# Performance work log

Hardware: AMD Instinct MI355X
Metric: run time of the kernel (lower is better)

Reference implementation:

```python
import jax, jax.numpy as jnp
import numpy as np

D_MODEL = 1024
NHEAD = 16
HEAD_DIM = D_MODEL // NHEAD
DFF = 4096
EPS = 1e-5


def _layernorm(x, g, b):
    mu = jnp.mean(x, axis=-1, keepdims=True)
    var = jnp.mean(jnp.square(x - mu), axis=-1, keepdims=True)
    return (x - mu) * jax.lax.rsqrt(var + EPS) * g + b


def setup_inputs() -> dict:
    key = jax.random.key(0)
    ks = jax.random.split(key, 20)
    B, S = 2, 2048
    s = 0.02
    inp = {
        "src": jax.random.normal(ks[0], (B, S, D_MODEL), jnp.float32),
        "recompute_idx": jnp.sort(jax.random.randint(ks[1], (409,), 0, S)),
        "cached_k": jax.random.normal(ks[2], (B, NHEAD, S, HEAD_DIM), jnp.float32),
        "cached_v": jax.random.normal(ks[3], (B, NHEAD, S, HEAD_DIM), jnp.float32),
        "Wq": jax.random.normal(ks[4], (D_MODEL, D_MODEL), jnp.float32) * s,
        "bq": jnp.zeros((D_MODEL,), jnp.float32),
        "Wk": jax.random.normal(ks[5], (D_MODEL, D_MODEL), jnp.float32) * s,
        "bk": jnp.zeros((D_MODEL,), jnp.float32),
        "Wv": jax.random.normal(ks[6], (D_MODEL, D_MODEL), jnp.float32) * s,
        "bv": jnp.zeros((D_MODEL,), jnp.float32),
        "Wo": jax.random.normal(ks[7], (D_MODEL, D_MODEL), jnp.float32) * s,
        "bo": jnp.zeros((D_MODEL,), jnp.float32),
        "W1": jax.random.normal(ks[8], (DFF, D_MODEL), jnp.float32) * s,
        "b1": jnp.zeros((DFF,), jnp.float32),
        "W2": jax.random.normal(ks[9], (D_MODEL, DFF), jnp.float32) * s,
        "b2": jnp.zeros((D_MODEL,), jnp.float32),
        "g1": jnp.ones((D_MODEL,), jnp.float32),
        "beta1": jnp.zeros((D_MODEL,), jnp.float32),
        "g2": jnp.ones((D_MODEL,), jnp.float32),
        "beta2": jnp.zeros((D_MODEL,), jnp.float32),
    }
    return inp


def reference(src, recompute_idx, cached_k, cached_v, Wq, bq, Wk, bk, Wv, bv,
              Wo, bo, W1, b1, W2, b2, g1, beta1, g2, beta2):
    B, S, D = src.shape
    H, hd = NHEAD, HEAD_DIM

    # Q for all tokens
    q = (src @ Wq.T + bq).reshape(B, S, H, hd).transpose(0, 2, 1, 3)  # [B,H,S,hd]

    # K/V recomputed only for selected tokens, scattered over cached KV
    src_rec = src[:, recompute_idx, :]  # [B,R,D]
    R = src_rec.shape[1]
    k_rec = (src_rec @ Wk.T + bk).reshape(B, R, H, hd).transpose(0, 2, 1, 3)
    v_rec = (src_rec @ Wv.T + bv).reshape(B, R, H, hd).transpose(0, 2, 1, 3)
    k_full = cached_k.at[:, :, recompute_idx, :].set(k_rec)  # [B,H,S,hd]
    v_full = cached_v.at[:, :, recompute_idx, :].set(v_rec)

    # attention over mixed cached/fresh KV
    scores = jnp.einsum('bhqd,bhkd->bhqk', q, k_full) / np.sqrt(hd).astype(src.dtype)
    probs = jax.nn.softmax(scores, axis=-1)
    attn = jnp.einsum('bhqk,bhkd->bhqd', probs, v_full)
    attn = attn.transpose(0, 2, 1, 3).reshape(B, S, D)
    attn = attn @ Wo.T + bo

    x = _layernorm(src + attn, g1, beta1)
    ff = jax.nn.relu(x @ W1.T + b1) @ W2.T + b2
    x = _layernorm(x + ff, g2, beta2)
    return x
```

## Files before the change

kernel.cpp:

```cpp
#include <hip/hip_runtime.h>
#include <hip/hip_bf16.h>

typedef __attribute__((ext_vector_type(4))) float f32x4;
typedef __attribute__((ext_vector_type(8))) short s16x8;
typedef __attribute__((ext_vector_type(4))) short s16x4;
typedef __attribute__((ext_vector_type(2))) short s16x2;

typedef __attribute__((address_space(1))) const unsigned int guint;
typedef __attribute__((address_space(3))) unsigned int luint;

#define D_MODEL 1024
#define NHEAD 16
#define HEAD_DIM 64
#define DFF 4096
#define SEQ 2048
#define BATCH 2
#define QSCALE 0.18033688011112042f

__device__ __forceinline__ float b2f(short s) {
  union { unsigned int u; float f; } v;
  v.u = ((unsigned int)(unsigned short)s) << 16;
  return v.f;
}
__device__ __forceinline__ short f2b(float f) {
  __hip_bfloat16 h = __float2bfloat16(f);
  return *reinterpret_cast<short*>(&h);
}
__device__ __forceinline__ s16x8 cvt8(f32x4 a, f32x4 b) {
  s16x8 r;
  #pragma unroll
  for (int i = 0; i < 4; ++i) { r[i] = f2b(a[i]); r[i + 4] = f2b(b[i]); }
  return r;
}

template<int MODE, int BN, bool AF32, bool WF32>
__global__ __launch_bounds__(256, 3)
void gemm_nt(const void* __restrict__ Av, const void* __restrict__ Wv,
             const float* __restrict__ bias, short* __restrict__ out,
             int M, int N, int K,
             const int* __restrict__ idx, int R,
             const float* __restrict__ bias2, const float* __restrict__ bias3,
             short* __restrict__ pB, short* __restrict__ pC,
             short* __restrict__ pD)
{
  constexpr bool GLDS = (!AF32 && !WF32);
  constexpr int NI = BN / 32;

  const float* Af = (const float*)Av;
  const short* Ab = (const short*)Av;
  const float* Wf = (const float*)Wv;
  const short* Wb = (const short*)Wv;

  const int tid  = threadIdx.x;
  const int lane = tid & 63, wave = tid >> 6;
  const int g = lane >> 4, l15 = lane & 15;
  const int wm = (wave & 1) * 64, wn = (wave >> 1) * (BN / 2);

  const int nwg = gridDim.x * gridDim.y;
  int lid = blockIdx.y * gridDim.x + blockIdx.x;
  if ((nwg & 7) == 0) lid = (lid & 7) * (nwg >> 3) + (lid >> 3);
  const int bn = lid % gridDim.x;
  const int bm0 = lid / gridDim.x;

  int task = 0, bm = bm0, Mt = M;
  if (MODE == 8) {
    if (bm0 < 32)      { task = 0; bm = bm0;      Mt = M; }
    else if (bm0 < 39) { task = 1; bm = bm0 - 32; Mt = BATCH * R; }
    else               { task = 2; bm = bm0 - 39; Mt = BATCH * R; }
  }

  f32x4 acc[4][NI] = {};

  if constexpr (GLDS) {
    __shared__ short As[2][128][32];
    __shared__ short Bs[2][BN][32];

    const short* Wbase = Wb + ((MODE == 8) ? ((size_t)task << 20) : 0);
    const int nz   = (MODE == 6) ? gridDim.z : 1;
    const int Keff = K / nz;
    const int kOff = (MODE == 6) ? (int)blockIdx.z * Keff : 0;

    const int rA0 = wave * 16 + (lane >> 2);
    const int rA1 = rA0 + 64;
    const int c0  = (lane & 3) * 8;

    auto arow = [&](int r) -> long {
      const int gm = bm * 128 + r;
      const int am = gm < Mt ? gm : Mt - 1;
      if (MODE == 8 && task > 0) {
        const int b0 = am / R;
        return (long)(b0 * SEQ + idx[am - b0 * R]);
      }
      return am;
    };
    const long aR0 = arow(rA0), aR1 = arow(rA1);
    const long wR0 = (long)bn * BN + rA0;

    const short* gA0 = Ab + aR0 * K + kOff + c0;
    const short* gA1 = Ab + aR1 * K + kOff + c0;
    const short* gB0 = Wbase + wR0 * K + kOff + c0;
    const short* gB1 = nullptr;
    if constexpr (BN == 128) gB1 = Wbase + ((long)bn * BN + rA1) * K + kOff + c0;

    auto stage = [&](int buf, int k0) {
      luint* lA0 = (luint*)((short*)As + buf * 4096 + wave * 512);
      luint* lA1 = (luint*)((short*)As + buf * 4096 + (4 + wave) * 512);
      luint* lB0 = (luint*)((short*)Bs + buf * (BN * 32) + wave * 512);
      __builtin_amdgcn_global_load_lds((guint*)(gA0 + k0), lA0, 16, 0, 0);
      __builtin_amdgcn_global_load_lds((guint*)(gA1 + k0), lA1, 16, 0, 0);
      __builtin_amdgcn_global_load_lds((guint*)(gB0 + k0), lB0, 16, 0, 0);
      if constexpr (BN == 128) {
        luint* lB1 = (luint*)((short*)Bs + buf * (BN * 32) + (4 + wave) * 512);
        __builtin_amdgcn_global_load_lds((guint*)(gB1 + k0), lB1, 16, 0, 0);
      }
    };

    stage(0, 0);
    __syncthreads();
    int cur = 0;
    for (int k0 = 0; k0 < Keff; k0 += 32) {
      const int k1 = k0 + 32;
      if (k1 < Keff) stage(cur ^ 1, k1);

      s16x8 af[4], bf4[NI];
      #pragma unroll
      for (int mi = 0; mi < 4; ++mi)
        af[mi] = *(const s16x8*)&As[cur][wm + mi * 16 + l15][g * 8];
      #pragma unroll
      for (int ni = 0; ni < NI; ++ni)
        bf4[ni] = *(const s16x8*)&Bs[cur][wn + ni * 16 + l15][g * 8];
      #pragma unroll
      for (int mi = 0; mi < 4; ++mi)
        #pragma unroll
        for (int ni = 0; ni < NI; ++ni)
          acc[mi][ni] = __builtin_amdgcn_mfma_f32_16x16x32_bf16(af[mi], bf4[ni], acc[mi][ni], 0, 0, 0);

      __syncthreads();
      cur ^= 1;
    }
  } else {
    __shared__ short As[128][40];
    __shared__ short Bs[128][40];
    const int r0 = tid >> 1, c0 = (tid & 1) * 16;
    const int gm0 = bm * 128 + r0;
    const int am0 = gm0 < M ? gm0 : M - 1;
    long aRow0;
    if (MODE == 3 || MODE == 4) {
      const int b0 = am0 / R;
      aRow0 = (long)(b0 * SEQ + idx[am0 - b0 * R]);
    } else {
      aRow0 = am0;
    }
    const long wRow0 = bn * 128 + r0;

    for (int k0 = 0; k0 < K; k0 += 32) {
      __syncthreads();
      if (AF32) {
        f32x4 a0 = *(const f32x4*)(Af + aRow0 * K + k0 + c0);
        f32x4 a1 = *(const f32x4*)(Af + aRow0 * K + k0 + c0 + 4);
        f32x4 a2 = *(const f32x4*)(Af + aRow0 * K + k0 + c0 + 8);
        f32x4 a3 = *(const f32x4*)(Af + aRow0 * K + k0 + c0 + 12);
        *(s16x8*)&As[r0][c0]     = cvt8(a0, a1);
        *(s16x8*)&As[r0][c0 + 8] = cvt8(a2, a3);
      } else {
        *(s16x8*)&As[r0][c0]     = *(const s16x8*)(Ab + aRow0 * K + k0 + c0);
        *(s16x8*)&As[r0][c0 + 8] = *(const s16x8*)(Ab + aRow0 * K + k0 + c0 + 8);
      }
      if (WF32) {
        f32x4 w0 = *(const f32x4*)(Wf + wRow0 * K + k0 + c0);
        f32x4 w1 = *(const f32x4*)(Wf + wRow0 * K + k0 + c0 + 4);
        f32x4 w2 = *(const f32x4*)(Wf + wRow0 * K + k0 + c0 + 8);
        f32x4 w3 = *(const f32x4*)(Wf + wRow0 * K + k0 + c0 + 12);
        *(s16x8*)&Bs[r0][c0]     = cvt8(w0, w1);
        *(s16x8*)&Bs[r0][c0 + 8] = cvt8(w2, w3);
      } else {
        *(s16x8*)&Bs[r0][c0]     = *(const s16x8*)(Wb + wRow0 * K + k0 + c0);
        *(s16x8*)&Bs[r0][c0 + 8] = *(const s16x8*)(Wb + wRow0 * K + k0 + c0 + 8);
      }
      __syncthreads();

      s16x8 af[4], bf4[4];
      #pragma unroll
      for (int mi = 0; mi < 4; ++mi)
        af[mi] = *(const s16x8*)&As[wm + mi * 16 + l15][g * 8];
      #pragma unroll
      for (int ni = 0; ni < 4; ++ni)
        bf4[ni] = *(const s16x8*)&Bs[wn + ni * 16 + l15][g * 8];
      #pragma unroll
      for (int mi = 0; mi < 4; ++mi)
        #pragma unroll
        for (int ni = 0; ni < 4; ++ni)
          acc[mi][ni % NI] = __builtin_amdgcn_mfma_f32_16x16x32_bf16(af[mi], bf4[ni], acc[mi][ni % NI], 0, 0, 0);
    }
  }

  short* outz = out;
  if (MODE == 6) {
    const int z = blockIdx.z;
    outz = (z == 0) ? out : (z == 1) ? pB : (z == 2) ? pC : pD;
  }

  #pragma unroll
  for (int mi = 0; mi < 4; ++mi) {
    #pragma unroll
    for (int ni = 0; ni < NI; ++ni) {
      const int gn = bn * BN + wn + ni * 16 + l15;
      float bv;
      if (MODE == 6)      bv = 0.f;
      else if (MODE == 8) bv = (task == 0) ? bias[gn] : (task == 1) ? bias2[gn] : bias3[gn];
      else                bv = bias[gn];
      #pragma unroll
      for (int r = 0; r < 4; ++r) {
        const int gm = bm * 128 + wm + mi * 16 + g * 4 + r;
        if (MODE == 8) { if (gm >= Mt) continue; }
        else           { if (gm >= M)  continue; }
        float v = acc[mi][ni][r] + bv;
        if (MODE == 1) v = v > 0.f ? v : 0.f;
        if (MODE == 2) v *= QSCALE;
        if (MODE == 0 || MODE == 1) {
          out[(long)gm * N + gn] = f2b(v);
        } else if (MODE == 2) {
          const int b = gm >> 11, s = gm & (SEQ - 1);
          const int h = gn >> 6, d = gn & 63;
          out[(((long)(b * NHEAD + h)) * SEQ + s) * 64 + d] = f2b(v);
        } else if (MODE == 3) {
          const int b = gm / R, s = idx[gm - b * R];
          const int h = gn >> 6, d = gn & 63;
          out[(((long)(b * NHEAD + h)) * SEQ + s) * 64 + d] = f2b(v);
        } else if (MODE == 4) {
          const int b = gm / R, s = idx[gm - b * R];
          const int h = gn >> 6, d = gn & 63;
          out[(((long)(b * NHEAD + h)) * 64 + d) * SEQ + s] = f2b(v);
        } else if (MODE == 6) {
          outz[(long)gm * N + gn] = f2b(v);
        } else {
          const int h = gn >> 6, d = gn & 63;
          if (task == 0) {
            const int b = gm >> 11, s = gm & (SEQ - 1);
            out[(((long)(b * NHEAD + h)) * SEQ + s) * 64 + d] = f2b(v * QSCALE);
          } else if (task == 1) {
            const int b = gm / R, s = idx[gm - b * R];
            (out + (1L << 22))[(((long)(b * NHEAD + h)) * SEQ + s) * 64 + d] = f2b(v);
          } else {
            const int b = gm / R, s = idx[gm - b * R];
            (out + (1L << 23))[(((long)(b * NHEAD + h)) * 64 + d) * SEQ + s] = f2b(v);
          }
        }
      }
    }
  }
}

__global__ __launch_bounds__(256, 2)
void attn_fwd(const short* __restrict__ Q, const short* __restrict__ Kf,
              const short* __restrict__ Vt, short* __restrict__ out)
{
  __shared__ short Kl[2][64][64];
  __shared__ short Vl[2][64][64];

  const int tid  = threadIdx.x;
  const int lane = tid & 63, w = tid >> 6;
  const int g = lane >> 4, l15 = lane & 15;
  const int bh = blockIdx.x;
  const int qt = blockIdx.y;
  const int b  = bh >> 4, h = bh & 15;

  const long base = (long)bh * SEQ * 64;
  const int  q0   = qt * 128 + w * 32;

  s16x8 qf[2][2];
  #pragma unroll
  for (int mi = 0; mi < 2; ++mi)
    #pragma unroll
    for (int c = 0; c < 2; ++c)
      qf[mi][c] = *(const s16x8*)(Q + base + (long)(q0 + mi * 16 + l15) * 64 + c * 32 + g * 8);

  f32x4 o[2][4] = {};
  f32x4 os[2] = {};

  s16x8 ones;
  #pragma unroll
  for (int j = 0; j < 8; ++j) ones[j] = (short)0x3F80;

  auto ldsw = [](short (*buf)[64], int row, int slot) -> short* {
    return (short*)((char*)&buf[0][0] + row * 128 + ((slot ^ (row & 7)) << 4));
  };

  const int bo0 = w * 2048 + lane * 16;
  const int bo1 = bo0 + 1024;
  const int row0 = bo0 >> 7, ss0 = (((bo0 >> 4) & 7) ^ (row0 & 7));
  const int row1 = bo1 >> 7, ss1 = (((bo1 >> 4) & 7) ^ (row1 & 7));
  const short* gK0 = Kf + base + row0 * 64 + ss0 * 8;
  const short* gK1 = Kf + base + row1 * 64 + ss1 * 8;
  const short* gV0 = Vt + base + (long)row0 * SEQ + ss0 * 8;
  const short* gV1 = Vt + base + (long)row1 * SEQ + ss1 * 8;

  auto stage = [&](int buf, int t) {
    char* kb8 = (char*)&Kl[buf][0][0] + w * 2048;
    char* vb8 = (char*)&Vl[buf][0][0] + w * 2048;
    __builtin_amdgcn_global_load_lds((guint*)(gK0 + t * 4096), (luint*)kb8, 16, 0, 0);
    __builtin_amdgcn_global_load_lds((guint*)(gK1 + t * 4096), (luint*)(kb8 + 1024), 16, 0, 0);
    __builtin_amdgcn_global_load_lds((guint*)(gV0 + t * 64), (luint*)vb8, 16, 0, 0);
    __builtin_amdgcn_global_load_lds((guint*)(gV1 + t * 64), (luint*)(vb8 + 1024), 16, 0, 0);
  };

  stage(0, 0);
  __syncthreads();
  int cur = 0;
  for (int t = 0; t < SEQ / 64; ++t) {
    if (t + 1 < SEQ / 64) stage(cur ^ 1, t + 1);

    f32x4 sc[2][4] = {};
    __builtin_amdgcn_s_setprio(1);
    #pragma unroll
    for (int c = 0; c < 2; ++c)
      #pragma unroll
      for (int n = 0; n < 4; ++n) {
        s16x8 kb = *(const s16x8*)ldsw(Kl[cur], n * 16 + l15, c * 4 + g);
        sc[0][n] = __builtin_amdgcn_mfma_f32_16x16x32_bf16(kb, qf[0][c], sc[0][n], 0, 0, 0);
        sc[1][n] = __builtin_amdgcn_mfma_f32_16x16x32_bf16(kb, qf[1][c], sc[1][n], 0, 0, 0);
      }
    __builtin_amdgcn_s_setprio(0);

    s16x8 pa[2][2];
    #pragma unroll
    for (int mi = 0; mi < 2; ++mi) {
      #pragma unroll
      for (int n = 0; n < 4; ++n)
        #pragma unroll
        for (int r = 0; r < 4; ++r) {
          float e;
          asm("v_exp_f32 %0, %1" : "=v"(e) : "v"(sc[mi][n][r]));
          sc[mi][n][r] = e;
        }
      unsigned int wpk[4][2];
      #pragma unroll
      for (int n = 0; n < 4; ++n)
        #pragma unroll
        for (int p = 0; p < 2; ++p)
          asm("v_cvt_pk_bf16_f32 %0, %1, %2"
              : "=v"(wpk[n][p]) : "v"(sc[mi][n][2 * p]), "v"(sc[mi][n][2 * p + 1]));
      #pragma unroll
      for (int c = 0; c < 2; ++c) {
        union { s16x8 v; unsigned int u[4]; } pu;
        #pragma unroll
        for (int p = 0; p < 2; ++p) {
          unsigned int a = wpk[2 * c][p], bb = wpk[2 * c + 1][p];
          asm volatile("v_permlane32_swap_b32 %0, %1" : "+v"(a), "+v"(bb));
          asm volatile("v_permlane16_swap_b32 %0, %1" : "+v"(a), "+v"(bb));
          pu.u[p]     = a;
          pu.u[2 + p] = bb;
        }
        pa[mi][c] = pu.v;
      }
    }

    __builtin_amdgcn_s_setprio(1);
    #pragma unroll
    for (int dt = 0; dt < 4; ++dt)
      #pragma unroll
      for (int c = 0; c < 2; ++c) {
        s16x8 vb = *(const s16x8*)ldsw(Vl[cur], dt * 16 + l15, c * 4 + g);
        o[0][dt] = __builtin_amdgcn_mfma_f32_16x16x32_bf16(pa[0][c], vb, o[0][dt], 0, 0, 0);
        o[1][dt] = __builtin_amdgcn_mfma_f32_16x16x32_bf16(pa[1][c], vb, o[1][dt], 0, 0, 0);
      }
    #pragma unroll
    for (int mi = 0; mi < 2; ++mi)
      #pragma unroll
      for (int c = 0; c < 2; ++c)
        os[mi] = __builtin_amdgcn_mfma_f32_16x16x32_bf16(pa[mi][c], ones, os[mi], 0, 0, 0);
    __builtin_amdgcn_s_setprio(0);

    __syncthreads();
    cur ^= 1;
  }

  float inv[2][4];
  #pragma unroll
  for (int mi = 0; mi < 2; ++mi)
    #pragma unroll
    for (int r = 0; r < 4; ++r)
      inv[mi][r] = 1.0f / os[mi][r];

  #pragma unroll
  for (int mi = 0; mi < 2; ++mi)
    #pragma unroll
    for (int dt = 0; dt < 4; ++dt)
      #pragma unroll
      for (int r = 0; r < 4; ++r) {
        const int q   = q0 + mi * 16 + g * 4 + r;
        const int col = h * 64 + dt * 16 + l15;
        out[((long)(b * SEQ + q)) * D_MODEL + col] = f2b(o[mi][dt][r] * inv[mi][r]);
      }
}

template<bool RES_F32, bool OUT_F32>
__global__ __launch_bounds__(256, 4)
void ln_ff2(const short* __restrict__ p0, const short* __restrict__ p1,
            const float* __restrict__ bias, const void* __restrict__ resv,
            const float* __restrict__ g, const float* __restrict__ beta,
            void* __restrict__ outv)
{
  __shared__ float red[8];
  const int row = blockIdx.x;
  const int tid = threadIdx.x;
  const int lane = tid & 63, w = tid >> 6;

  s16x4 v0 = *(const s16x4*)(p0 + (long)row * D_MODEL + tid * 4);
  s16x4 v1 = *(const s16x4*)(p1 + (long)row * D_MODEL + tid * 4);
  f32x4 vb = *(const f32x4*)(bias + tid * 4);
  float x[4];
  if (RES_F32) {
    f32x4 vr = *(const f32x4*)((const float*)resv + (long)row * D_MODEL + tid * 4);
    #pragma unroll
    for (int i = 0; i < 4; ++i) x[i] = vr[i] + b2f(v0[i]) + b2f(v1[i]) + vb[i];
  } else {
    s16x4 vr = *(const s16x4*)((const short*)resv + (long)row * D_MODEL + tid * 4);
    #pragma unroll
    for (int i = 0; i < 4; ++i) x[i] = b2f(vr[i]) + b2f(v0[i]) + b2f(v1[i]) + vb[i];
  }

  float sum = x[0] + x[1] + x[2] + x[3];
  #pragma unroll
  for (int msk = 32; msk >= 1; msk >>= 1) sum += __shfl_xor(sum, msk, 64);
  if (lane == 0) red[w] = sum;
  __syncthreads();
  sum = red[0] + red[1] + red[2] + red[3];
  const float mu = sum * (1.f / D_MODEL);

  float sq = 0.f;
  #pragma unroll
  for (int i = 0; i < 4; ++i) { float d = x[i] - mu; sq += d * d; }
  #pragma unroll
  for (int msk = 32; msk >= 1; msk >>= 1) sq += __shfl_xor(sq, msk, 64);
  if (lane == 0) red[4 + w] = sq;
  __syncthreads();
  sq = red[4] + red[5] + red[6] + red[7];
  const float rs = rsqrtf(sq * (1.f / D_MODEL) + 1e-5f);

  if (OUT_F32) {
    f32x4 ov;
    #pragma unroll
    for (int i = 0; i < 4; ++i) {
      const int c = tid * 4 + i;
      ov[i] = (x[i] - mu) * rs * g[c] + beta[c];
    }
    *(f32x4*)((float*)outv + (long)row * D_MODEL + tid * 4) = ov;
  } else {
    s16x4 ov;
    #pragma unroll
    for (int i = 0; i < 4; ++i) {
      const int c = tid * 4 + i;
      ov[i] = f2b((x[i] - mu) * rs * g[c] + beta[c]);
    }
    *(s16x4*)((short*)outv + (long)row * D_MODEL + tid * 4) = ov;
  }
}

__global__ __launch_bounds__(256, 4)
void ln_ff4(const short* __restrict__ p0, const short* __restrict__ p1,
            const short* __restrict__ p2, const short* __restrict__ p3,
            const float* __restrict__ bias, const short* __restrict__ xres,
            const float* __restrict__ g, const float* __restrict__ beta,
            float* __restrict__ outv)
{
  __shared__ float red[8];
  const int row = blockIdx.x;
  const int tid = threadIdx.x;
  const int lane = tid & 63, w = tid >> 6;

  s16x4 v0 = *(const s16x4*)(p0 + (long)row * D_MODEL + tid * 4);
  s16x4 v1 = *(const s16x4*)(p1 + (long)row * D_MODEL + tid * 4);
  s16x4 v2 = *(const s16x4*)(p2 + (long)row * D_MODEL + tid * 4);
  s16x4 v3 = *(const s16x4*)(p3 + (long)row * D_MODEL + tid * 4);
  s16x4 vx = *(const s16x4*)(xres + (long)row * D_MODEL + tid * 4);
  f32x4 vb = *(const f32x4*)(bias + tid * 4);
  float x[4];
  #pragma unroll
  for (int i = 0; i < 4; ++i)
    x[i] = b2f(vx[i]) + b2f(v0[i]) + b2f(v1[i]) + b2f(v2[i]) + b2f(v3[i]) + vb[i];

  float sum = x[0] + x[1] + x[2] + x[3];
  #pragma unroll
  for (int msk = 32; msk >= 1; msk >>= 1) sum += __shfl_xor(sum, msk, 64);
  if (lane == 0) red[w] = sum;
  __syncthreads();
  sum = red[0] + red[1] + red[2] + red[3];
  const float mu = sum * (1.f / D_MODEL);

  float sq = 0.f;
  #pragma unroll
  for (int i = 0; i < 4; ++i) { float d = x[i] - mu; sq += d * d; }
  #pragma unroll
  for (int msk = 32; msk >= 1; msk >>= 1) sq += __shfl_xor(sq, msk, 64);
  if (lane == 0) red[4 + w] = sq;
  __syncthreads();
  sq = red[4] + red[5] + red[6] + red[7];
  const float rs = rsqrtf(sq * (1.f / D_MODEL) + 1e-5f);

  f32x4 ov;
  #pragma unroll
  for (int i = 0; i < 4; ++i) {
    const int c = tid * 4 + i;
    ov[i] = (x[i] - mu) * rs * g[c] + beta[c];
  }
  *(f32x4*)(outv + (long)row * D_MODEL + tid * 4) = ov;
}

template<bool RES_F32, bool OUT_F32>
__global__ __launch_bounds__(256, 4)
void ln_res(const short* __restrict__ a, const void* __restrict__ resv,
            const float* __restrict__ g, const float* __restrict__ beta,
            void* __restrict__ outv)
{
  __shared__ float red[8];
  const int row = blockIdx.x;
  const int tid = threadIdx.x;
  const int lane = tid & 63, w = tid >> 6;

  s16x4 va = *(const s16x4*)(a + (long)row * D_MODEL + tid * 4);
  float x[4];
  if (RES_F32) {
    f32x4 vr = *(const f32x4*)((const float*)resv + (long)row * D_MODEL + tid * 4);
    #pragma unroll
    for (int i = 0; i < 4; ++i) x[i] = b2f(va[i]) + vr[i];
  } else {
    s16x4 vr = *(const s16x4*)((const short*)resv + (long)row * D_MODEL + tid * 4);
    #pragma unroll
    for (int i = 0; i < 4; ++i) x[i] = b2f(va[i]) + b2f(vr[i]);
  }
  float sum = x[0] + x[1] + x[2] + x[3];
  #pragma unroll
  for (int msk = 32; msk >= 1; msk >>= 1) sum += __shfl_xor(sum, msk, 64);
  if (lane == 0) red[w] = sum;
  __syncthreads();
  sum = red[0] + red[1] + red[2] + red[3];
  const float mu = sum * (1.f / D_MODEL);

  float sq = 0.f;
  #pragma unroll
  for (int i = 0; i < 4; ++i) { float d = x[i] - mu; sq += d * d; }
  #pragma unroll
  for (int msk = 32; msk >= 1; msk >>= 1) sq += __shfl_xor(sq, msk, 64);
  if (lane == 0) red[4 + w] = sq;
  __syncthreads();
  sq = red[4] + red[5] + red[6] + red[7];
  const float rs = rsqrtf(sq * (1.f / D_MODEL) + 1e-5f);

  if (OUT_F32) {
    f32x4 ov;
    #pragma unroll
    for (int i = 0; i < 4; ++i) {
      const int c = tid * 4 + i;
      ov[i] = (x[i] - mu) * rs * g[c] + beta[c];
    }
    *(f32x4*)((float*)outv + (long)row * D_MODEL + tid * 4) = ov;
  } else {
    s16x4 ov;
    #pragma unroll
    for (int i = 0; i < 4; ++i) {
      const int c = tid * 4 + i;
      ov[i] = f2b((x[i] - mu) * rs * g[c] + beta[c]);
    }
    *(s16x4*)((short*)outv + (long)row * D_MODEL + tid * 4) = ov;
  }
}

__global__ void cvt_all(const float* __restrict__ ck, const float* __restrict__ cv,
                        const float* __restrict__ src,
                        const float* __restrict__ Wq, const float* __restrict__ Wk,
                        const float* __restrict__ Wv, const float* __restrict__ Wo,
                        const float* __restrict__ W1, const float* __restrict__ W2,
                        short* __restrict__ k_ws, short* __restrict__ v_ws,
                        short* __restrict__ srcb,
                        short* __restrict__ Wqb, short* __restrict__ W1b,
                        short* __restrict__ W2b)
{
  for (int i = blockIdx.x * blockDim.x + threadIdx.x; i < 5767168;
       i += gridDim.x * blockDim.x) {
    if (i >= 5242880) {
      const int j = i - 5242880;
      const int bh = j >> 14;
      const int rem = j & 16383;
      const int d = rem & 63;
      const int s0 = (rem >> 6) << 3;
      s16x8 r;
      #pragma unroll
      for (int k = 0; k < 8; ++k)
        r[k] = f2b(cv[((long)bh * SEQ + s0 + k) * 64 + d]);
      *(s16x8*)(v_ws + ((long)bh * 64 + d) * SEQ + s0) = r;
      continue;
    }
    const float* s; short* d; int li;
    if      (i < 1048576) { s = ck;  d = k_ws;           li = i; }
    else if (i < 2097152) { s = src; d = srcb;           li = i - 1048576; }
    else if (i < 2359296) { s = Wq;  d = Wqb;            li = i - 2097152; }
    else if (i < 2621440) { s = Wk;  d = Wqb + 1048576;  li = i - 2359296; }
    else if (i < 2883584) { s = Wv;  d = Wqb + 2097152;  li = i - 2621440; }
    else if (i < 3145728) { s = Wo;  d = Wqb + 3145728;  li = i - 2883584; }
    else if (i < 4194304) { s = W1;  d = W1b;            li = i - 3145728; }
    else                  { s = W2;  d = W2b;            li = i - 4194304; }
    f32x4 v = *(const f32x4*)(s + (long)li * 4);
    s16x4 r;
    #pragma unroll
    for (int j = 0; j < 4; ++j) r[j] = f2b(v[j]);
    *(s16x4*)(d + (long)li * 4) = r;
  }
}

__global__ void cvt_v_t(const float* __restrict__ in, short* __restrict__ out)
{
  const int c2 = blockIdx.x * blockDim.x + threadIdx.x;
  const int bh = c2 >> 14;
  const int rem = c2 & 16383;
  const int d = rem & 63;
  const int s0 = (rem >> 6) << 3;
  s16x8 r;
  #pragma unroll
  for (int j = 0; j < 8; ++j)
    r[j] = f2b(in[((long)bh * SEQ + s0 + j) * 64 + d]);
  *(s16x8*)(out + ((long)bh * 64 + d) * SEQ + s0) = r;
}

__global__ void cvt_f32_bf16(const f32x4* __restrict__ in, s16x4* __restrict__ out, int n4)
{
  for (int i = blockIdx.x * blockDim.x + threadIdx.x; i < n4; i += gridDim.x * blockDim.x) {
    f32x4 v = in[i];
    s16x4 r;
    #pragma unroll
    for (int j = 0; j < 4; ++j) r[j] = f2b(v[j]);
    out[i] = r;
  }
}

extern "C" void kernel_launch(void* const* d_in, const int* in_sizes, int n_in,
                              void* d_out, int out_size, void* d_ws, size_t ws_size,
                              hipStream_t stream)
{
  const float* src = (const float*)d_in[0];
  const int*   idx = (const int*)  d_in[1];
  const float* ck  = (const float*)d_in[2];
  const float* cv  = (const float*)d_in[3];
  const float* Wq  = (const float*)d_in[4];
  const float* bq  = (const float*)d_in[5];
  const float* Wk  = (const float*)d_in[6];
  const float* bk  = (const float*)d_in[7];
  const float* Wv  = (const float*)d_in[8];
  const float* bv  = (const float*)d_in[9];
  const float* Wo  = (const float*)d_in[10];
  const float* bo  = (const float*)d_in[11];
  const float* W1  = (const float*)d_in[12];
  const float* b1  = (const float*)d_in[13];
  const float* W2  = (const float*)d_in[14];
  const float* b2  = (const float*)d_in[15];
  const float* g1  = (const float*)d_in[16];
  const float* be1 = (const float*)d_in[17];
  const float* g2  = (const float*)d_in[18];
  const float* be2 = (const float*)d_in[19];
  float* out = (float*)d_out;

  char* ws = (char*)d_ws;
  const size_t SZ = (size_t)4096 * 1024 * 2;
  short* x_ws    = (short*)(ws);
  short* proj_ws = (short*)(ws + SZ);
  short* q_ws    = (short*)(ws + 2 * SZ);
  short* k_ws    = (short*)(ws + 3 * SZ);
  short* v_ws    = (short*)(ws + 4 * SZ);
  short* attn_ws = (short*)(ws + 5 * SZ);
  short* h_ws    = (short*)(ws + 2 * SZ);
  short* W1b     = (short*)(ws + 6 * SZ);
  short* W2b     = (short*)(ws + 7 * SZ);
  short* srcb    = (short*)(ws + 8 * SZ);
  short* Wqb     = (short*)(ws + 9 * SZ);
  const bool big = ws_size >= 10 * SZ;

  const int M = BATCH * SEQ;
  const int R = 409;
  const int Mr = BATCH * R;
  const int nkv4 = BATCH * NHEAD * SEQ * HEAD_DIM / 4;

  if (big) {
    cvt_all<<<2048, 256, 0, stream>>>(ck, cv, src, Wq, Wk, Wv, Wo, W1, W2,
                                      k_ws, v_ws, srcb, Wqb, W1b, W2b);
    gemm_nt<8, 64, false, false><<<dim3(16, 46), 256, 0, stream>>>(
        srcb, Wqb, bq, q_ws, M, 1024, 1024, idx, R, bk, bv, nullptr, nullptr, nullptr);
    attn_fwd<<<dim3(BATCH * NHEAD, SEQ / 128), 256, 0, stream>>>(q_ws, k_ws, v_ws, attn_ws);
    gemm_nt<6, 64, false, false><<<dim3(16, 32, 2), 256, 0, stream>>>(
        attn_ws, Wqb + 3145728, nullptr, proj_ws, M, 1024, 1024, nullptr, 0,
        nullptr, nullptr, q_ws, nullptr, nullptr);
    ln_ff2<true, false><<<4096, 256, 0, stream>>>(proj_ws, q_ws, bo, src, g1, be1, x_ws);
    gemm_nt<1, 128, false, false><<<dim3(32, 32), 256, 0, stream>>>(
        x_ws, W1b, b1, h_ws, M, DFF, 1024, nullptr, 0, nullptr, nullptr,
        nullptr, nullptr, nullptr);
    gemm_nt<6, 128, false, false><<<dim3(8, 32, 4), 256, 0, stream>>>(
        h_ws, W2b, nullptr, proj_ws, M, 1024, 4096, nullptr, 0,
        nullptr, nullptr, W1b, srcb, Wqb);
    ln_ff4<<<4096, 256, 0, stream>>>(proj_ws, W1b, srcb, Wqb, b2, x_ws, g2, be2, out);
  } else {
    cvt_f32_bf16<<<2048, 256, 0, stream>>>((const f32x4*)ck, (s16x4*)k_ws, nkv4);
    cvt_v_t<<<2048, 256, 0, stream>>>(cv, v_ws);
    gemm_nt<2, 128, true, true><<<dim3(8, 32), 256, 0, stream>>>(
        src, Wq, bq, q_ws, M, 1024, 1024, nullptr, 0, nullptr, nullptr, nullptr, nullptr, nullptr);
    gemm_nt<3, 128, true, true><<<dim3(8, 7), 256, 0, stream>>>(
        src, Wk, bk, k_ws, Mr, 1024, 1024, idx, R, nullptr, nullptr, nullptr, nullptr, nullptr);
    gemm_nt<4, 128, true, true><<<dim3(8, 7), 256, 0, stream>>>(
        src, Wv, bv, v_ws, Mr, 1024, 1024, idx, R, nullptr, nullptr, nullptr, nullptr, nullptr);
    attn_fwd<<<dim3(BATCH * NHEAD, SEQ / 128), 256, 0, stream>>>(q_ws, k_ws, v_ws, attn_ws);
    gemm_nt<0, 128, false, true><<<dim3(8, 32), 256, 0, stream>>>(
        attn_ws, Wo, bo, proj_ws, M, 1024, 1024, nullptr, 0, nullptr, nullptr, nullptr, nullptr, nullptr);
    ln_res<true, false><<<4096, 256, 0, stream>>>(proj_ws, src, g1, be1, x_ws);
    gemm_nt<1, 128, false, true><<<dim3(32, 32), 256, 0, stream>>>(
        x_ws, W1, b1, h_ws, M, DFF, 1024, nullptr, 0, nullptr, nullptr, nullptr, nullptr, nullptr);
    gemm_nt<0, 128, false, true><<<dim3(8, 32), 256, 0, stream>>>(
        h_ws, W2, b2, proj_ws, M, 1024, DFF, nullptr, 0, nullptr, nullptr, nullptr, nullptr, nullptr);
    ln_res<false, true><<<4096, 256, 0, stream>>>(proj_ws, x_ws, g2, be2, out);
  }
}
```

Measured before the change: 236.9 us.

## Swizzle GEMM LDS tiles and use partial vmcnt waits for double-buffer prefetch

In the GEMM kernel the global-to-LDS column placement is XOR-swizzled and the MFMA fragment reads use the matching swizzled column, so LDS reads should hit fewer bank conflicts. In both the GEMM and attention loops, the full __syncthreads after each prefetch is replaced by an explicit s_waitcnt vmcnt(N) plus s_barrier. Only the current tile's loads are waited on, while the next tile's loads stay in flight during compute. This relies on exact counts of outstanding loads per thread; a wrong count would give stale-data races.

```diff
diff --git a/kernel.cpp b/kernel.cpp
--- a/kernel.cpp
+++ b/kernel.cpp
@@ -82,7 +82,7 @@
 
     const int rA0 = wave * 16 + (lane >> 2);
     const int rA1 = rA0 + 64;
-    const int c0  = (lane & 3) * 8;
+    const int cs = (((lane & 3) ^ ((lane >> 3) & 3)) * 8);
 
     auto arow = [&](int r) -> long {
       const int gm = bm * 128 + r;
@@ -96,11 +96,11 @@
     const long aR0 = arow(rA0), aR1 = arow(rA1);
     const long wR0 = (long)bn * BN + rA0;
 
-    const short* gA0 = Ab + aR0 * K + kOff + c0;
-    const short* gA1 = Ab + aR1 * K + kOff + c0;
-    const short* gB0 = Wbase + wR0 * K + kOff + c0;
+    const short* gA0 = Ab + aR0 * K + kOff + cs;
+    const short* gA1 = Ab + aR1 * K + kOff + cs;
+    const short* gB0 = Wbase + wR0 * K + kOff + cs;
     const short* gB1 = nullptr;
-    if constexpr (BN == 128) gB1 = Wbase + ((long)bn * BN + rA1) * K + kOff + c0;
+    if constexpr (BN == 128) gB1 = Wbase + ((long)bn * BN + rA1) * K + kOff + cs;
 
     auto stage = [&](int buf, int k0) {
       luint* lA0 = (luint*)((short*)As + buf * 4096 + wave * 512);
@@ -115,27 +115,37 @@
       }
     };
 
+    const int rcol = ((g ^ ((l15 >> 1) & 3)) * 8);
+
+    const int nt = Keff / 32;
     stage(0, 0);
-    __syncthreads();
     int cur = 0;
-    for (int k0 = 0; k0 < Keff; k0 += 32) {
-      const int k1 = k0 + 32;
-      if (k1 < Keff) stage(cur ^ 1, k1);
+    for (int t = 0; t < nt; ++t) {
+      if (t + 1 < nt) {
+        stage(cur ^ 1, (t + 1) * 32);
+        if constexpr (BN == 128) asm volatile("s_waitcnt vmcnt(4)" ::: "memory");
+        else                     asm volatile("s_waitcnt vmcnt(3)" ::: "memory");
+      } else {
+        asm volatile("s_waitcnt vmcnt(0)" ::: "memory");
+      }
+      __builtin_amdgcn_s_barrier();
+      __builtin_amdgcn_sched_barrier(0);
 
       s16x8 af[4], bf4[NI];
       #pragma unroll
       for (int mi = 0; mi < 4; ++mi)
-        af[mi] = *(const s16x8*)&As[cur][wm + mi * 16 + l15][g * 8];
+        af[mi] = *(const s16x8*)&As[cur][wm + mi * 16 + l15][rcol];
       #pragma unroll
       for (int ni = 0; ni < NI; ++ni)
-        bf4[ni] = *(const s16x8*)&Bs[cur][wn + ni * 16 + l15][g * 8];
+        bf4[ni] = *(const s16x8*)&Bs[cur][wn + ni * 16 + l15][rcol];
       #pragma unroll
       for (int mi = 0; mi < 4; ++mi)
         #pragma unroll
         for (int ni = 0; ni < NI; ++ni)
           acc[mi][ni] = __builtin_amdgcn_mfma_f32_16x16x32_bf16(af[mi], bf4[ni], acc[mi][ni], 0, 0, 0);
 
-      __syncthreads();
+      __builtin_amdgcn_sched_barrier(0);
+      __builtin_amdgcn_s_barrier();
       cur ^= 1;
     }
   } else {
@@ -305,10 +315,16 @@
   };
 
   stage(0, 0);
-  __syncthreads();
   int cur = 0;
   for (int t = 0; t < SEQ / 64; ++t) {
-    if (t + 1 < SEQ / 64) stage(cur ^ 1, t + 1);
+    if (t + 1 < SEQ / 64) {
+      stage(cur ^ 1, t + 1);
+      asm volatile("s_waitcnt vmcnt(4)" ::: "memory");
+    } else {
+      asm volatile("s_waitcnt vmcnt(0)" ::: "memory");
+    }
+    __builtin_amdgcn_s_barrier();
+    __builtin_amdgcn_sched_barrier(0);
 
     f32x4 sc[2][4] = {};
     __builtin_amdgcn_s_setprio(1);
@@ -371,7 +387,8 @@
         os[mi] = __builtin_amdgcn_mfma_f32_16x16x32_bf16(pa[mi][c], ones, os[mi], 0, 0, 0);
     __builtin_amdgcn_s_setprio(0);
 
-    __syncthreads();
+    __builtin_amdgcn_sched_barrier(0);
+    __builtin_amdgcn_s_barrier();
     cur ^= 1;
   }
 
```

New measurement: 238.9 us. Within noise of the previous version (+0.8%).
